# Kernel optimization log

Hardware: AMD Instinct MI355X
Metric: run time of the kernel (lower is better)

The kernel has to match this reference:

```python
import jax, jax.numpy as jnp
from jax import lax
import numpy as np

NUM_CHANNELS = 64
NUM_WEIGHTS = 31
VMIN, VMAX = -1.0, 1.0
INIT_SCALE = 1.0


def setup_inputs() -> dict:
    key = jax.random.key(0)
    kx, = jax.random.split(key, 1)
    x = jax.random.normal(kx, (16, NUM_CHANNELS, 128, 128), dtype=jnp.float32)
    # faithful 'linear' init: w[c, j] = mu_j * init_scale, tiled over channels
    mus = np.linspace(VMIN, VMAX, NUM_WEIGHTS, dtype=np.float32)
    weights = jnp.asarray(np.tile(mus[None, :] * INIT_SCALE, (NUM_CHANNELS, 1)))
    return {"x": x, "weights": weights}


def _rbf_act(x_r, weights, vmin, vmax):
    # x_r: [C, M], weights: [C, K]
    K = weights.shape[1]
    mus = jnp.linspace(vmin, vmax, K, dtype=x_r.dtype)        # RBF centers
    sigma = (vmax - vmin) / (K - 1)                           # optox RbfAct sigma
    inv_2s2 = 1.0 / (2.0 * sigma * sigma)

    def body(acc, wm):
        w, mu = wm                                            # w: [C]
        phi = jnp.exp(-(x_r - mu) ** 2 * inv_2s2)             # [C, M]
        return acc + w[:, None] * phi, None

    out, _ = lax.scan(body, jnp.zeros_like(x_r), (weights.T, mus))
    return out


def reference(x, weights):
    # x: [N, C, H, W] -> [C, N, H, W] -> [C, N*H*W] (group == 1)
    xt = jnp.swapaxes(x, 0, 1)
    shp = xt.shape
    x_r = xt.reshape(shp[0], -1)
    y = _rbf_act(x_r, weights, VMIN, VMAX)
    return jnp.swapaxes(y.reshape(shp), 0, 1)
```

## Files before the change

### kernel.cpp

```cpp
#include <hip/hip_runtime.h>


constexpr int KW   = 31;
constexpr int R    = 3;
constexpr int TAB  = KW + 2 * R;
constexpr int TN   = 1024;
#define U0      -5.0f
#define U1      35.0f
#define HU      ((U1 - U0) / (TN - 1))
#define INV_HU  ((TN - 1) / (U1 - U0))
#define TSCALE  (15.0f * INV_HU)
#define TBIAS   (20.0f * INV_HU)

#define LOG2E   1.44269504089f
#define SQ_C    0.84932180028f

#if defined(__has_builtin) && __has_builtin(__builtin_amdgcn_exp2f)
#define FAST_EXP2(a) __builtin_amdgcn_exp2f(a)
#else
#define FAST_EXP2(a) exp2f(a)
#endif

__global__ __launch_bounds__(256) void rbf_act_kernel(
    const float* __restrict__ x,
    const float* __restrict__ w,
    float* __restrict__ y)
{
    __shared__ float lw[TAB];
    __shared__ float tbl[TN];
    const int bid = blockIdx.x;
    const int tid = threadIdx.x;
    const int c = (bid >> 2) & 63;
    if (tid < TAB) {
        const int j = tid - R;
        lw[tid] = (j >= 0 && j < KW) ? w[c * KW + j] : 0.0f;
    }
    __syncthreads();

    const float C0 = 1.0f;
    const float C1 = 0.60653065971f;
    const float C2 = 0.13533528324f;
    const float C3 = 0.01110899654f;
    const float C4 = 3.35462628e-4f;
    const float C5 = 3.72665317e-6f;
    const float C6 = 1.52299797e-8f;

    #pragma unroll
    for (int kk = 0; kk < TN / 256; ++kk) {
        const int idx = tid + kk * 256;
        const float u = U0 + (float)idx * HU;
        float j0f = __builtin_rintf(u);
        j0f = fminf(fmaxf(j0f, 0.0f), 30.0f);
        const int j0 = (int)j0f;
        const float dup = (u - j0f) + 3.0f;
        const float r  = FAST_EXP2(LOG2E * dup);
        const float t  = SQ_C * dup;
        const float g  = FAST_EXP2(-t * t);
        const float r2 = r * r;
        const float r3 = r2 * r;
        const float r4 = r2 * r2;
        const float r5 = r3 * r2;
        const float r6 = r3 * r3;
        const float* wp = lw + j0;
        float acc;
        acc = wp[0] * C0;
        acc = __builtin_fmaf(wp[1] * C1, r,  acc);
        acc = __builtin_fmaf(wp[2] * C2, r2, acc);
        acc = __builtin_fmaf(wp[3] * C3, r3, acc);
        acc = __builtin_fmaf(wp[4] * C4, r4, acc);
        acc = __builtin_fmaf(wp[5] * C5, r5, acc);
        acc = __builtin_fmaf(wp[6] * C6, r6, acc);
        tbl[idx] = g * acc;
    }
    __syncthreads();

    const size_t base = (size_t)bid * 4096;
    const float4* __restrict__ xv = (const float4*)(x + base);
    float4*       __restrict__ yv = (float4*)(y + base);

    #pragma unroll
    for (int i = 0; i < 4; ++i) {
        float4 v = xv[tid + i * 256];
        float4 o;
        float* vp = (float*)&v;
        float* op = (float*)&o;
        #pragma unroll
        for (int e = 0; e < 4; ++e) {
            float t = __builtin_fmaf(vp[e], TSCALE, TBIAS);
            t = fminf(fmaxf(t, 0.0f), (float)(TN - 1) - 0.001f);
            const float fi = __builtin_truncf(t);
            const float f  = t - fi;
            const int   i0 = (int)fi;
            const float y0 = tbl[i0];
            const float y1 = tbl[i0 + 1];
            op[e] = __builtin_fmaf(f, y1 - y0, y0);
        }
        yv[tid + i * 256] = o;
    }
}

extern "C" void kernel_launch(void* const* d_in, const int* in_sizes, int n_in,
                              void* d_out, int out_size, void* d_ws, size_t ws_size,
                              hipStream_t stream) {
    const float* x = (const float*)d_in[0];
    const float* w = (const float*)d_in[1];
    float*       y = (float*)d_out;
    const int total   = in_sizes[0];
    const int nblocks = total / 4096;
    rbf_act_kernel<<<nblocks, 256, 0, stream>>>(x, w, y);
}
```

Baseline: 110.9 us.

## Prefetch inputs before table build, double per-block work, use nontemporal stores

Each block now handles 8192 elements instead of 4096 and issues all eight vector loads of x before building the per-channel lookup table, so global load latency overlaps the table computation. The weight staging through shared memory and its barrier are removed; each table entry instead reads its seven weights directly from global memory with clamped indices. Output stores use nontemporal hints. In exchange, register pressure rises from holding 32 input floats per thread, the block count is halved, and redundant global weight reads increase.

```diff
diff --git a/kernel.cpp b/kernel.cpp
--- a/kernel.cpp
+++ b/kernel.cpp
@@ -1,10 +1,8 @@
 #include <hip/hip_runtime.h>
 
 
-constexpr int KW   = 31;
-constexpr int R    = 3;
-constexpr int TAB  = KW + 2 * R;
-constexpr int TN   = 1024;
+constexpr int KW = 31;
+constexpr int TN = 1024;
 #define U0      -5.0f
 #define U1      35.0f
 #define HU      ((U1 - U0) / (TN - 1))
@@ -21,21 +19,25 @@
 #define FAST_EXP2(a) exp2f(a)
 #endif
 
+typedef float vfloat4 __attribute__((ext_vector_type(4)));
+
 __global__ __launch_bounds__(256) void rbf_act_kernel(
     const float* __restrict__ x,
     const float* __restrict__ w,
     float* __restrict__ y)
 {
-    __shared__ float lw[TAB];
     __shared__ float tbl[TN];
     const int bid = blockIdx.x;
     const int tid = threadIdx.x;
-    const int c = (bid >> 2) & 63;
-    if (tid < TAB) {
-        const int j = tid - R;
-        lw[tid] = (j >= 0 && j < KW) ? w[c * KW + j] : 0.0f;
-    }
-    __syncthreads();
+    const int c = (bid >> 1) & 63;
+
+    const size_t base = (size_t)bid * 8192;
+    const vfloat4* __restrict__ xv = (const vfloat4*)(x + base);
+    vfloat4*       __restrict__ yv = (vfloat4*)(y + base);
+
+    vfloat4 v[8];
+    #pragma unroll
+    for (int i = 0; i < 8; ++i) v[i] = xv[tid + i * 256];
 
     const float C0 = 1.0f;
     const float C1 = 0.60653065971f;
@@ -44,7 +46,7 @@
     const float C4 = 3.35462628e-4f;
     const float C5 = 3.72665317e-6f;
     const float C6 = 1.52299797e-8f;
-
+    const float* __restrict__ wr = w + c * KW;
     #pragma unroll
     for (int kk = 0; kk < TN / 256; ++kk) {
         const int idx = tid + kk * 256;
@@ -61,41 +63,42 @@
         const float r4 = r2 * r2;
         const float r5 = r3 * r2;
         const float r6 = r3 * r3;
-        const float* wp = lw + j0;
+        float wv[7];
+        #pragma unroll
+        for (int k = 0; k < 7; ++k) {
+            const int jj = j0 - 3 + k;
+            const int jc = min(max(jj, 0), KW - 1);
+            const float wj = wr[jc];
+            wv[k] = (jj == jc) ? wj : 0.0f;
+        }
         float acc;
-        acc = wp[0] * C0;
-        acc = __builtin_fmaf(wp[1] * C1, r,  acc);
-        acc = __builtin_fmaf(wp[2] * C2, r2, acc);
-        acc = __builtin_fmaf(wp[3] * C3, r3, acc);
-        acc = __builtin_fmaf(wp[4] * C4, r4, acc);
-        acc = __builtin_fmaf(wp[5] * C5, r5, acc);
-        acc = __builtin_fmaf(wp[6] * C6, r6, acc);
+        acc = wv[0] * C0;
+        acc = __builtin_fmaf(wv[1] * C1, r,  acc);
+        acc = __builtin_fmaf(wv[2] * C2, r2, acc);
+        acc = __builtin_fmaf(wv[3] * C3, r3, acc);
+        acc = __builtin_fmaf(wv[4] * C4, r4, acc);
+        acc = __builtin_fmaf(wv[5] * C5, r5, acc);
+        acc = __builtin_fmaf(wv[6] * C6, r6, acc);
         tbl[idx] = g * acc;
     }
     __syncthreads();
 
-    const size_t base = (size_t)bid * 4096;
-    const float4* __restrict__ xv = (const float4*)(x + base);
-    float4*       __restrict__ yv = (float4*)(y + base);
-
     #pragma unroll
-    for (int i = 0; i < 4; ++i) {
-        float4 v = xv[tid + i * 256];
-        float4 o;
-        float* vp = (float*)&v;
-        float* op = (float*)&o;
+    for (int i = 0; i < 8; ++i) {
+        vfloat4 vv = v[i];
+        vfloat4 o;
         #pragma unroll
         for (int e = 0; e < 4; ++e) {
-            float t = __builtin_fmaf(vp[e], TSCALE, TBIAS);
+            float t = __builtin_fmaf(vv[e], TSCALE, TBIAS);
             t = fminf(fmaxf(t, 0.0f), (float)(TN - 1) - 0.001f);
             const float fi = __builtin_truncf(t);
             const float f  = t - fi;
             const int   i0 = (int)fi;
             const float y0 = tbl[i0];
             const float y1 = tbl[i0 + 1];
-            op[e] = __builtin_fmaf(f, y1 - y0, y0);
+            o[e] = __builtin_fmaf(f, y1 - y0, y0);
         }
-        yv[tid + i * 256] = o;
+        __builtin_nontemporal_store(o, &yv[tid + i * 256]);
     }
 }
 
@@ -106,6 +109,6 @@
     const float* w = (const float*)d_in[1];
     float*       y = (float*)d_out;
     const int total   = in_sizes[0];
-    const int nblocks = total / 4096;
+    const int nblocks = total / 8192;
     rbf_act_kernel<<<nblocks, 256, 0, stream>>>(x, w, y);
 }
```

New measurement: 109.7 us. About the same (-1.0%).
